# Performance work log

Hardware: AMD Instinct MI355X
Metric: run time of the kernel (lower is better)

The kernel has to match this reference:

```python
import jax, jax.numpy as jnp
import numpy as np

D_MODEL = 1024
D_STATE = 16
D_CONV = 4
EXPAND = 2
DT_RANK = 64
D_INNER = EXPAND * D_MODEL  # 2048
BATCH = 2
SEQ = 1024


def _silu(v):
    return v * jax.nn.sigmoid(v)


def setup_inputs() -> dict:
    key = jax.random.key(0)
    ks = jax.random.split(key, 8)
    x = jax.random.normal(ks[0], (BATCH, SEQ, D_MODEL), dtype=jnp.float32)
    W_in = jax.random.normal(ks[1], (2 * D_INNER, D_MODEL), dtype=jnp.float32) * (D_MODEL ** -0.5)
    conv_w = jax.random.normal(ks[2], (D_INNER, 1, D_CONV), dtype=jnp.float32) * (D_CONV ** -0.5)
    conv_b = jnp.zeros((D_INNER,), dtype=jnp.float32)
    W_x = jax.random.normal(ks[3], (DT_RANK + 2 * D_STATE, D_INNER), dtype=jnp.float32) * (D_INNER ** -0.5)
    W_dt = jax.random.uniform(ks[4], (D_INNER, DT_RANK), minval=-(DT_RANK ** -0.5), maxval=DT_RANK ** -0.5, dtype=jnp.float32)
    # dt bias init: inverse-softplus of dt sampled log-uniform in [1e-3, 1e-1]
    dt = jnp.exp(jax.random.uniform(ks[5], (D_INNER,), dtype=jnp.float32) * (np.log(0.1) - np.log(0.001)) + np.log(0.001))
    dt = jnp.clip(dt, 1e-4)
    b_dt = dt + jnp.log(-jnp.expm1(-dt))
    # A_log init: log of 1..d_state tiled per channel (S4D-real)
    A_log = jnp.log(jnp.tile(jnp.arange(1, D_STATE + 1, dtype=jnp.float32), (D_INNER, 1)))
    D = jnp.ones((D_INNER,), dtype=jnp.float32)
    W_out = jax.random.normal(ks[6], (D_MODEL, D_INNER), dtype=jnp.float32) * (D_INNER ** -0.5)
    return {"x": x, "W_in": W_in, "conv_w": conv_w, "conv_b": conv_b, "W_x": W_x,
            "W_dt": W_dt, "b_dt": b_dt, "A_log": A_log, "D": D, "W_out": W_out}


def _selective_scan(u, dt, A, B_in, C_in, D):
    # u, dt: [B,L,d_inner]; B_in, C_in: [B,L,d_state]; A: [d_inner,d_state]; D: [d_inner]
    Bsz = u.shape[0]

    def step(h, inp):
        u_t, dt_t, B_t, C_t = inp  # [B,d_inner], [B,d_inner], [B,d_state], [B,d_state]
        dA = jnp.exp(dt_t[:, :, None] * A)                     # [B,d_inner,d_state]
        h = dA * h + dt_t[:, :, None] * B_t[:, None, :] * u_t[:, :, None]
        y = jnp.einsum('bds,bs->bd', h, C_t)
        return h, y

    h0 = jnp.zeros((Bsz, D_INNER, D_STATE), dtype=u.dtype)
    xs = (u.transpose(1, 0, 2), dt.transpose(1, 0, 2),
          B_in.transpose(1, 0, 2), C_in.transpose(1, 0, 2))
    _, ys = jax.lax.scan(step, h0, xs)                          # ys: [L,B,d_inner]
    return ys.transpose(1, 0, 2) + u * D


def reference(x, W_in, conv_w, conv_b, W_x, W_dt, b_dt, A_log, D, W_out):
    # in_proj and gate split
    xz = x @ W_in.T                                            # [B,T,2*d_inner]
    x_in, z = jnp.split(xz, 2, axis=-1)
    # depthwise causal conv1d (left-pad d_conv-1, same as pad-both + slice :T)
    xi = x_in.transpose(0, 2, 1)                               # [B,d_inner,T]
    conv = jax.lax.conv_general_dilated(xi, conv_w, window_strides=(1,),
                                        padding=[(D_CONV - 1, 0)],
                                        feature_group_count=D_INNER)
    x_act = _silu(conv + conv_b[None, :, None]).transpose(0, 2, 1)  # [B,T,d_inner]
    # dt / B / C projections
    dbc = x_act @ W_x.T
    dt_lr, B_in, C_in = jnp.split(dbc, [DT_RANK, DT_RANK + D_STATE], axis=-1)
    dt = jax.nn.softplus(dt_lr @ W_dt.T + b_dt)                # [B,T,d_inner]
    A = -jnp.exp(A_log)                                        # [d_inner,d_state]
    y = _selective_scan(x_act, dt, A, B_in, C_in, D)
    y = y * _silu(z)
    return y @ W_out.T
```

## Files before the change

kernel.cpp:

```cpp
#include <hip/hip_runtime.h>
#include <math.h>

#define D_MODEL 1024
#define D_STATE 16
#define D_CONV  4
#define DT_RANK 64
#define D_INNER 2048
#define BATCH   2
#define SEQ     1024
#define BT      (BATCH*SEQ)
#define KSPLIT  16

typedef int   v4i __attribute__((ext_vector_type(4)));
typedef float v4f __attribute__((ext_vector_type(4)));
typedef short s8v __attribute__((ext_vector_type(8)));
typedef unsigned short u16;

template<int BM, int BN, int BK, int TM, int TN, int EPI>
__launch_bounds__(256)
__global__ void gemm_nt(const float* __restrict__ A, int lda,
                        const float* __restrict__ B, int ldb,
                        float* __restrict__ C, int ldc,
                        int K, const float* __restrict__ bias) {
    constexpr int BX = BN / TN;
    constexpr int BY = BM / TM;
    constexpr int THREADS = BX * BY;

    __shared__ float As[BK][BM + 1];
    __shared__ float Bs[BK][BN + 1];

    const int tid = threadIdx.x;
    const int tx  = tid % BX;
    const int ty  = tid / BX;
    const int m0  = blockIdx.y * BM;
    const int n0  = blockIdx.x * BN;

    float acc[TM][TN] = {};

    for (int k0 = 0; k0 < K; k0 += BK) {
        #pragma unroll
        for (int l = 0; l < (BM * BK) / (THREADS * 4); ++l) {
            int idx = (tid + l * THREADS) * 4;
            int row = idx / BK, col = idx % BK;
            const float4 v = *reinterpret_cast<const float4*>(
                &A[(size_t)(m0 + row) * lda + k0 + col]);
            As[col + 0][row] = v.x; As[col + 1][row] = v.y;
            As[col + 2][row] = v.z; As[col + 3][row] = v.w;
        }
        #pragma unroll
        for (int l = 0; l < (BN * BK) / (THREADS * 4); ++l) {
            int idx = (tid + l * THREADS) * 4;
            int row = idx / BK, col = idx % BK;
            const float4 v = *reinterpret_cast<const float4*>(
                &B[(size_t)(n0 + row) * ldb + k0 + col]);
            Bs[col + 0][row] = v.x; Bs[col + 1][row] = v.y;
            Bs[col + 2][row] = v.z; Bs[col + 3][row] = v.w;
        }
        __syncthreads();

        #pragma unroll
        for (int kk = 0; kk < BK; ++kk) {
            float a[TM], b[TN];
            #pragma unroll
            for (int i = 0; i < TM; ++i) a[i] = As[kk][ty * TM + i];
            #pragma unroll
            for (int j = 0; j < TN; ++j) b[j] = Bs[kk][tx * TN + j];
            #pragma unroll
            for (int i = 0; i < TM; ++i)
                #pragma unroll
                for (int j = 0; j < TN; ++j)
                    acc[i][j] = fmaf(a[i], b[j], acc[i][j]);
        }
        __syncthreads();
    }

    #pragma unroll
    for (int i = 0; i < TM; ++i) {
        float* outp = &C[(size_t)(m0 + ty * TM + i) * ldc + n0 + tx * TN];
        float vals[4];
        #pragma unroll
        for (int j = 0; j < TN; ++j) {
            float val = acc[i][j];
            if (EPI == 1) {
                val += bias[n0 + tx * TN + j];
                val = (val > 20.f) ? val : log1pf(expf(val));
            }
            vals[j] = val;
        }
        float4 v;
        v.x = vals[0]; v.y = vals[1]; v.z = vals[2]; v.w = vals[3];
        *reinterpret_cast<float4*>(outp) = v;
    }
}

template<int BM, int BN, int BK, int TM, int TN>
__launch_bounds__(128)
__global__ void gemm_nt_splitk(const float* __restrict__ A, int lda,
                               const float* __restrict__ B, int ldb,
                               float* __restrict__ part, int N, int kchunk) {
    constexpr int BX = BN / TN;
    constexpr int BY = BM / TM;
    constexpr int THREADS = BX * BY;

    __shared__ float As[BK][BM + 1];
    __shared__ float Bs[BK][BN + 1];

    const int tid = threadIdx.x;
    const int tx  = tid % BX;
    const int ty  = tid / BX;
    const int m0  = blockIdx.y * BM;
    const int n0  = blockIdx.x * BN;
    const int kb  = blockIdx.z * kchunk;

    float acc[TM][TN] = {};

    for (int k0 = kb; k0 < kb + kchunk; k0 += BK) {
        #pragma unroll
        for (int l = 0; l < (BM * BK) / (THREADS * 4); ++l) {
            int idx = (tid + l * THREADS) * 4;
            int row = idx / BK, col = idx % BK;
            const float4 v = *reinterpret_cast<const float4*>(
                &A[(size_t)(m0 + row) * lda + k0 + col]);
            As[col + 0][row] = v.x; As[col + 1][row] = v.y;
            As[col + 2][row] = v.z; As[col + 3][row] = v.w;
        }
        #pragma unroll
        for (int l = 0; l < (BN * BK) / (THREADS * 4); ++l) {
            int idx = (tid + l * THREADS) * 4;
            int row = idx / BK, col = idx % BK;
            const float4 v = *reinterpret_cast<const float4*>(
                &B[(size_t)(n0 + row) * ldb + k0 + col]);
            Bs[col + 0][row] = v.x; Bs[col + 1][row] = v.y;
            Bs[col + 2][row] = v.z; Bs[col + 3][row] = v.w;
        }
        __syncthreads();

        #pragma unroll
        for (int kk = 0; kk < BK; ++kk) {
            float a[TM], b[TN];
            #pragma unroll
            for (int i = 0; i < TM; ++i) a[i] = As[kk][ty * TM + i];
            #pragma unroll
            for (int j = 0; j < TN; ++j) b[j] = Bs[kk][tx * TN + j];
            #pragma unroll
            for (int i = 0; i < TM; ++i)
                #pragma unroll
                for (int j = 0; j < TN; ++j)
                    acc[i][j] = fmaf(a[i], b[j], acc[i][j]);
        }
        __syncthreads();
    }

    float* base = part + (size_t)blockIdx.z * BT * N;
    #pragma unroll
    for (int i = 0; i < TM; ++i) {
        float* outp = &base[(size_t)(m0 + ty * TM + i) * N + n0 + tx * TN];
        float4 v;
        v.x = acc[i][0]; v.y = acc[i][1]; v.z = acc[i][2]; v.w = acc[i][3];
        *reinterpret_cast<float4*>(outp) = v;
    }
}

__global__ void reduce_splitk(const float* __restrict__ part,
                              float* __restrict__ outp, int n) {
    const int idx = blockIdx.x * 256 + threadIdx.x;
    if (idx >= n) return;
    float s = 0.f;
    #pragma unroll
    for (int kc = 0; kc < KSPLIT; ++kc)
        s += part[(size_t)kc * n + idx];
    outp[idx] = s;
}

__device__ __forceinline__ u16 rne_bf16(float x) {
    unsigned int u = __float_as_uint(x);
    unsigned int r = u + 0x7FFFu + ((u >> 16) & 1u);
    return (u16)(r >> 16);
}
__device__ __forceinline__ float bf2f(u16 h) {
    return __uint_as_float((unsigned int)h << 16);
}

__global__ void prep_kernel(const float* __restrict__ x,
                            const float* __restrict__ Win,
                            const float* __restrict__ Wout,
                            u16* __restrict__ xh,
                            u16* __restrict__ winh, u16* __restrict__ wouth) {
    const size_t M2 = 2u * 1024u * 1024u;
    size_t i = ((size_t)blockIdx.x * 256 + threadIdx.x) * 8;
    const float* src;
    u16* dst;
    size_t j;
    if (i < M2)            { src = x;    dst = xh;    j = i; }
    else if (i < 3 * M2)   { src = Win;  dst = winh;  j = i - M2; }
    else                   { src = Wout; dst = wouth; j = i - 3 * M2; }
    float4 a = *reinterpret_cast<const float4*>(&src[j]);
    float4 b = *reinterpret_cast<const float4*>(&src[j + 4]);
    float xs[8] = {a.x, a.y, a.z, a.w, b.x, b.y, b.z, b.w};
    unsigned int hw[4];
    #pragma unroll
    for (int q = 0; q < 4; ++q)
        hw[q] = (unsigned int)rne_bf16(xs[2*q]) | ((unsigned int)rne_bf16(xs[2*q+1]) << 16);
    *reinterpret_cast<v4i*>(&dst[j]) = *reinterpret_cast<v4i*>(hw);
}

template<int BM, int BN, int WM, int WN, int CBF16>
__launch_bounds__(256)
__global__ void gemm_bf16(const u16* __restrict__ Ahi, int lda,
                          const u16* __restrict__ Bhi, int ldb,
                          void* __restrict__ Cp, int ldc, int K) {
    constexpr int ACH = BM / 64;
    constexpr int BCH = BN / 64;
    constexpr int WMF = WM / 16;
    constexpr int WNF = WN / 16;
    constexpr int SA  = BM * 40;
    constexpr int SB  = BN * 40;
    constexpr int BUFSZ = SA + SB;
    constexpr int WCOLS = BN / WN;

    __shared__ u16 smem[2 * BUFSZ];

    const int tid  = threadIdx.x;
    const int lane = tid & 63;
    const int wave = tid >> 6;
    const int wr   = wave / WCOLS, wc = wave % WCOLS;
    const int m0   = blockIdx.y * BM, n0 = blockIdx.x * BN;

    size_t aBase[ACH]; int aW[ACH];
    #pragma unroll
    for (int q = 0; q < ACH; ++q) {
        int c = tid + q * 256, row = c >> 2, slot = c & 3;
        aBase[q] = (size_t)(m0 + row) * lda + slot * 8;
        aW[q] = row * 40 + slot * 8;
    }
    size_t bBase[BCH]; int bW[BCH];
    #pragma unroll
    for (int q = 0; q < BCH; ++q) {
        int c = tid + q * 256, row = c >> 2, slot = c & 3;
        bBase[q] = (size_t)(n0 + row) * ldb + slot * 8;
        bW[q] = row * 40 + slot * 8;
    }

    const int fr = lane & 15;
    const int fk = (lane >> 4) * 8;
    const int fq = lane >> 4;
    int aOff[WMF], bOff[WNF];
    #pragma unroll
    for (int i = 0; i < WMF; ++i) aOff[i] = (wr * WM + i * 16 + fr) * 40 + fk;
    #pragma unroll
    for (int j = 0; j < WNF; ++j) bOff[j] = (wc * WN + j * 16 + fr) * 40 + fk;

    v4f acc[WMF][WNF];
    #pragma unroll
    for (int i = 0; i < WMF; ++i)
        #pragma unroll
        for (int j = 0; j < WNF; ++j)
            acc[i][j] = (v4f)0.f;

    v4i rA[ACH], rB[BCH];

    auto loadg = [&](int k0) {
        #pragma unroll
        for (int q = 0; q < ACH; ++q)
            rA[q] = *reinterpret_cast<const v4i*>(Ahi + aBase[q] + k0);
        #pragma unroll
        for (int q = 0; q < BCH; ++q)
            rB[q] = *reinterpret_cast<const v4i*>(Bhi + bBase[q] + k0);
    };
    auto writelds = [&](u16* buf) {
        #pragma unroll
        for (int q = 0; q < ACH; ++q)
            *reinterpret_cast<v4i*>(&buf[aW[q]]) = rA[q];
        #pragma unroll
        for (int q = 0; q < BCH; ++q)
            *reinterpret_cast<v4i*>(&buf[SA + bW[q]]) = rB[q];
    };

    const int NK = K / 32;
    loadg(0);
    writelds(smem);
    if (NK > 1) loadg(32);
    __syncthreads();

    for (int k = 0; k < NK; ++k) {
        u16* cur = smem + (k & 1) * BUFSZ;
        if (k + 1 < NK) {
            writelds(smem + ((k + 1) & 1) * BUFSZ);
            if (k + 2 < NK) loadg((k + 2) * 32);
        }

        s8v ah[WMF];
        #pragma unroll
        for (int i = 0; i < WMF; ++i)
            ah[i] = *reinterpret_cast<const s8v*>(&cur[aOff[i]]);
        #pragma unroll
        for (int j = 0; j < WNF; ++j) {
            const s8v bh = *reinterpret_cast<const s8v*>(&cur[SA + bOff[j]]);
            #pragma unroll
            for (int i = 0; i < WMF; ++i)
                acc[i][j] = __builtin_amdgcn_mfma_f32_16x16x32_bf16(ah[i], bh, acc[i][j], 0, 0, 0);
        }
        __syncthreads();
    }

    #pragma unroll
    for (int i = 0; i < WMF; ++i) {
        const int row = m0 + wr * WM + i * 16 + fq * 4;
        #pragma unroll
        for (int j = 0; j < WNF; ++j) {
            const int col = n0 + wc * WN + j * 16 + fr;
            #pragma unroll
            for (int r = 0; r < 4; ++r) {
                if constexpr (CBF16) {
                    ((u16*)Cp)[(size_t)(row + r) * ldc + col] = rne_bf16(acc[i][j][r]);
                } else {
                    ((float*)Cp)[(size_t)(row + r) * ldc + col] = acc[i][j][r];
                }
            }
        }
    }
}

template<int INBF16>
__global__ void conv_silu_kernel(const void* __restrict__ x_in, int xld,
                                 const float* __restrict__ w,
                                 const float* __restrict__ b,
                                 float* __restrict__ x_act) {
    const int idx = blockIdx.x * blockDim.x + threadIdx.x;
    const int ch4 = (idx * 4) % D_INNER;
    const int m   = (idx * 4) / D_INNER;
    const int t   = m % SEQ;

    float4 wrow[4];
    #pragma unroll
    for (int c = 0; c < 4; ++c)
        wrow[c] = *reinterpret_cast<const float4*>(&w[(ch4 + c) * D_CONV]);
    float4 acc = *reinterpret_cast<const float4*>(&b[ch4]);

    #pragma unroll
    for (int j = 0; j < D_CONV; ++j) {
        const int tt = t - (D_CONV - 1) + j;
        if (tt >= 0) {
            float xi[4];
            if (INBF16) {
                const ushort4 v = *reinterpret_cast<const ushort4*>(
                    &((const u16*)x_in)[(size_t)(m - (D_CONV - 1) + j) * xld + ch4]);
                xi[0] = bf2f(v.x); xi[1] = bf2f(v.y);
                xi[2] = bf2f(v.z); xi[3] = bf2f(v.w);
            } else {
                const float4 v = *reinterpret_cast<const float4*>(
                    &((const float*)x_in)[(size_t)(m - (D_CONV - 1) + j) * xld + ch4]);
                xi[0] = v.x; xi[1] = v.y; xi[2] = v.z; xi[3] = v.w;
            }
            acc.x = fmaf(((const float*)&wrow[0])[j], xi[0], acc.x);
            acc.y = fmaf(((const float*)&wrow[1])[j], xi[1], acc.y);
            acc.z = fmaf(((const float*)&wrow[2])[j], xi[2], acc.z);
            acc.w = fmaf(((const float*)&wrow[3])[j], xi[3], acc.w);
        }
    }
    acc.x = acc.x / (1.f + __expf(-acc.x));
    acc.y = acc.y / (1.f + __expf(-acc.y));
    acc.z = acc.z / (1.f + __expf(-acc.z));
    acc.w = acc.w / (1.f + __expf(-acc.w));
    *reinterpret_cast<float4*>(&x_act[(size_t)idx * 4]) = acc;
}

template<int NC>
__launch_bounds__(256)
__global__ void scan_part1(const float* __restrict__ dt,
                           const float* __restrict__ x_act,
                           const float* __restrict__ dbc,
                           const float* __restrict__ A_log,
                           float* __restrict__ P, float* __restrict__ F) {
    constexpr int CL = SEQ / NC;
    __shared__ float Bsh[CL][D_STATE];
    const int tid = threadIdx.x;
    const int d = blockIdx.x * 256 + tid;
    const int c = blockIdx.y;
    const int b = blockIdx.z;
    const int mbase = b * SEQ + c * CL;

    {
        const int s = tid & 15, t0 = tid >> 4;
        #pragma unroll
        for (int q = 0; q < CL / 16; ++q)
            Bsh[t0 + 16 * q][s] = dbc[(size_t)(mbase + t0 + 16 * q) * 96 + DT_RANK + s];
    }
    float A[16];
    #pragma unroll
    for (int q = 0; q < 4; ++q) {
        float4 v = *reinterpret_cast<const float4*>(&A_log[d * 16 + q * 4]);
        A[q*4+0] = -__expf(v.x); A[q*4+1] = -__expf(v.y);
        A[q*4+2] = -__expf(v.z); A[q*4+3] = -__expf(v.w);
    }
    __syncthreads();

    float h[16] = {};
    float Pp[16];
    #pragma unroll
    for (int s = 0; s < 16; ++s) Pp[s] = 1.f;

    for (int t = 0; t < CL; ++t) {
        const int m = mbase + t;
        const float dtv = dt[(size_t)m * D_INNER + d];
        const float u   = x_act[(size_t)m * D_INNER + d];
        const float du  = dtv * u;
        float Bv[16];
        #pragma unroll
        for (int q = 0; q < 4; ++q) {
            float4 v = *reinterpret_cast<const float4*>(&Bsh[t][q * 4]);
            Bv[q*4+0] = v.x; Bv[q*4+1] = v.y; Bv[q*4+2] = v.z; Bv[q*4+3] = v.w;
        }
        #pragma unroll
        for (int s = 0; s < 16; ++s) {
            const float dA = __expf(dtv * A[s]);
            Pp[s] *= dA;
            h[s] = fmaf(dA, h[s], du * Bv[s]);
        }
    }
    const size_t base = ((size_t)(b * NC + c) * 16) * D_INNER + d;
    #pragma unroll
    for (int s = 0; s < 16; ++s) {
        P[base + (size_t)s * D_INNER] = Pp[s];
        F[base + (size_t)s * D_INNER] = h[s];
    }
}

template<int NC>
__launch_bounds__(256, 2)
__global__ void scan_combine(const float* __restrict__ P, float* F) {
    const int idx = blockIdx.x * 256 + threadIdx.x;
    const int d  = idx % D_INNER;
    const int bs = idx / D_INNER;
    const int b  = bs >> 4, s = bs & 15;
    const size_t base0 = ((size_t)b * NC * 16 + s) * D_INNER + d;
    const size_t cstep = (size_t)16 * D_INNER;

    float Pv[NC], Fv[NC];
    #pragma unroll
    for (int c = 0; c < NC; ++c) {
        Pv[c] = P[base0 + c * cstep];
        Fv[c] = F[base0 + c * cstep];
    }
    float G = 0.f;
    #pragma unroll
    for (int c = 0; c < NC; ++c) {
        const float f = Fv[c];
        Fv[c] = G;
        G = fmaf(Pv[c], G, f);
    }
    #pragma unroll
    for (int c = 0; c < NC; ++c)
        F[base0 + c * cstep] = Fv[c];
}

template<int NC, int ZBF16, int BF16OUT>
__launch_bounds__(256)
__global__ void scan_part2(const float* __restrict__ dt,
                           const float* __restrict__ x_act,
                           const float* __restrict__ dbc,
                           const float* __restrict__ A_log,
                           const float* __restrict__ Dp,
                           const float* __restrict__ Ginit,
                           const void* zp, int zld,
                           float* yf, u16* yh) {
    constexpr int CL = SEQ / NC;
    __shared__ float BCs[CL][32];
    const int tid = threadIdx.x;
    const int d = blockIdx.x * 256 + tid;
    const int c = blockIdx.y;
    const int b = blockIdx.z;
    const int mbase = b * SEQ + c * CL;

    {
        const int t0 = tid >> 3;
        const int j  = (tid & 7) * 4;
        if (t0 < CL) {
            float4 v = *reinterpret_cast<const float4*>(
                &dbc[(size_t)(mbase + t0) * 96 + DT_RANK + j]);
            *reinterpret_cast<float4*>(&BCs[t0][j]) = v;
        }
    }
    float A[16];
    #pragma unroll
    for (int q = 0; q < 4; ++q) {
        float4 v = *reinterpret_cast<const float4*>(&A_log[d * 16 + q * 4]);
        A[q*4+0] = -__expf(v.x); A[q*4+1] = -__expf(v.y);
        A[q*4+2] = -__expf(v.z); A[q*4+3] = -__expf(v.w);
    }
    float h[16];
    const size_t gbase = ((size_t)(b * NC + c) * 16) * D_INNER + d;
    #pragma unroll
    for (int s = 0; s < 16; ++s) h[s] = Ginit[gbase + (size_t)s * D_INNER];
    const float Dv = Dp[d];
    __syncthreads();

    for (int half = 0; half < 2; ++half) {
        const int tb = half * (CL / 2);
        float zreg[CL / 2];
        #pragma unroll
        for (int t = 0; t < CL / 2; ++t) {
            if (ZBF16)
                zreg[t] = bf2f(((const u16*)zp)[(size_t)(mbase + tb + t) * zld + d]);
            else
                zreg[t] = ((const float*)zp)[(size_t)(mbase + tb + t) * zld + d];
        }

        for (int t = 0; t < CL / 2; ++t) {
            const int m = mbase + tb + t;
            const float dtv = dt[(size_t)m * D_INNER + d];
            const float u   = x_act[(size_t)m * D_INNER + d];
            const float du  = dtv * u;
            float Bv[16], Cv[16];
            #pragma unroll
            for (int q = 0; q < 4; ++q) {
                float4 vb = *reinterpret_cast<const float4*>(&BCs[tb + t][q * 4]);
                float4 vc = *reinterpret_cast<const float4*>(&BCs[tb + t][16 + q * 4]);
                Bv[q*4+0] = vb.x; Bv[q*4+1] = vb.y; Bv[q*4+2] = vb.z; Bv[q*4+3] = vb.w;
                Cv[q*4+0] = vc.x; Cv[q*4+1] = vc.y; Cv[q*4+2] = vc.z; Cv[q*4+3] = vc.w;
            }
            float y0 = 0.f, y1 = 0.f;
            #pragma unroll
            for (int s = 0; s < 16; s += 2) {
                const float dA0 = __expf(dtv * A[s]);
                const float dA1 = __expf(dtv * A[s + 1]);
                h[s]     = fmaf(dA0, h[s],     du * Bv[s]);
                h[s + 1] = fmaf(dA1, h[s + 1], du * Bv[s + 1]);
                y0 = fmaf(h[s],     Cv[s],     y0);
                y1 = fmaf(h[s + 1], Cv[s + 1], y1);
            }
            float y = y0 + y1;
            y = fmaf(u, Dv, y);
            const float zv = zreg[t];
            const float g  = zv / (1.f + __expf(-zv));
            const float val = y * g;
            if (BF16OUT) {
                yh[(size_t)m * D_INNER + d] = rne_bf16(val);
            } else {
                yf[(size_t)m * D_INNER + d] = val;
            }
        }
    }
}

extern "C" void kernel_launch(void* const* d_in, const int* in_sizes, int n_in,
                              void* d_out, int out_size, void* d_ws, size_t ws_size,
                              hipStream_t stream) {
    const float* x      = (const float*)d_in[0];
    const float* W_in   = (const float*)d_in[1];
    const float* conv_w = (const float*)d_in[2];
    const float* conv_b = (const float*)d_in[3];
    const float* W_x    = (const float*)d_in[4];
    const float* W_dt   = (const float*)d_in[5];
    const float* b_dt   = (const float*)d_in[6];
    const float* A_log  = (const float*)d_in[7];
    const float* Dp     = (const float*)d_in[8];
    const float* W_out  = (const float*)d_in[9];
    float* out = (float*)d_out;

    const size_t M1 = 1024u * 1024u;
    const size_t fXACT = 4 * M1, fDBC = (size_t)BT * 96, fDT = 4 * M1;
    const size_t fPF32 = 2 * M1;
    const size_t fPF64 = 4 * M1;
    const size_t shorts = 20 * M1;
    const size_t need32 = (fXACT + fDBC + fDT + 2 * fPF32) * 4 + shorts * 2;
    const size_t need64 = (fXACT + fDBC + fDT + 2 * fPF64) * 4 + shorts * 2;

    if (ws_size >= need32) {
        const bool big = (ws_size >= need64);
        const size_t fPF = big ? fPF64 : fPF32;

        float* ws    = (float*)d_ws;
        float* x_act = ws;
        float* dbc   = x_act + fXACT;
        float* dtbuf = dbc   + fDBC;
        float* Pbuf  = dtbuf + fDT;
        float* Fbuf  = Pbuf  + fPF;
        u16* xh    = (u16*)(Fbuf + fPF);
        u16* winh  = xh    + 2 * M1;
        u16* wouth = winh  + 4 * M1;
        u16* xz    = wouth + 2 * M1;
        u16* yh    = xz    + 8 * M1;
        float* dbc_part = Pbuf;

        prep_kernel<<<dim3((8 * M1) / 2048), 256, 0, stream>>>(
            x, W_in, W_out, xh, winh, wouth);

        gemm_bf16<128, 128, 64, 64, 1><<<dim3(4096 / 128, BT / 128), 256, 0, stream>>>(
            xh, D_MODEL, winh, D_MODEL, xz, 4096, D_MODEL);

        conv_silu_kernel<1><<<dim3((BT * D_INNER) / 1024), 256, 0, stream>>>(
            xz, 4096, conv_w, conv_b, x_act);

        gemm_nt_splitk<64,32,16,4,4><<<dim3(96 / 32, BT / 64, KSPLIT), 128, 0, stream>>>(
            x_act, D_INNER, W_x, D_INNER, dbc_part, 96, D_INNER / KSPLIT);
        reduce_splitk<<<dim3((BT * 96 + 255) / 256), 256, 0, stream>>>(
            dbc_part, dbc, BT * 96);

        gemm_nt<64,64,16,4,4,1><<<dim3(D_INNER / 64, BT / 64), 256, 0, stream>>>(
            dbc, 96, W_dt, DT_RANK, dtbuf, D_INNER, DT_RANK, b_dt);

        if (big) {
            scan_part1<64><<<dim3(D_INNER / 256, 64, BATCH), 256, 0, stream>>>(
                dtbuf, x_act, dbc, A_log, Pbuf, Fbuf);
            scan_combine<64><<<dim3((BATCH * 16 * D_INNER) / 256), 256, 0, stream>>>(
                Pbuf, Fbuf);
            scan_part2<64, 1, 1><<<dim3(D_INNER / 256, 64, BATCH), 256, 0, stream>>>(
                dtbuf, x_act, dbc, A_log, Dp, Fbuf, xz + D_INNER, 4096,
                nullptr, yh);
        } else {
            scan_part1<32><<<dim3(D_INNER / 256, 32, BATCH), 256, 0, stream>>>(
                dtbuf, x_act, dbc, A_log, Pbuf, Fbuf);
            scan_combine<32><<<dim3((BATCH * 16 * D_INNER) / 256), 256, 0, stream>>>(
                Pbuf, Fbuf);
            scan_part2<32, 1, 1><<<dim3(D_INNER / 256, 32, BATCH), 256, 0, stream>>>(
                dtbuf, x_act, dbc, A_log, Dp, Fbuf, xz + D_INNER, 4096,
                nullptr, yh);
        }

        gemm_bf16<64, 128, 32, 64, 0><<<dim3(D_MODEL / 128, BT / 64), 256, 0, stream>>>(
            yh, D_INNER, wouth, D_INNER, out, D_MODEL, D_INNER);
    } else {
        float* ws    = (float*)d_ws;
        float* x_in  = ws;
        float* z     = x_in  + (size_t)BT * D_INNER;
        float* x_act = z     + (size_t)BT * D_INNER;
        float* dbc   = x_act + (size_t)BT * D_INNER;
        float* Pbuf  = dbc   + (size_t)BT * 96;
        float* Fbuf  = Pbuf  + (size_t)BATCH * 32 * 16 * D_INNER;
        float* dtbuf = x_in;
        float* yf    = z;

        gemm_nt<64,64,16,4,4,0><<<dim3(D_INNER/64, BT/64), 256, 0, stream>>>(
            x, D_MODEL, W_in, D_MODEL, x_in, D_INNER, D_MODEL, nullptr);
        gemm_nt<64,64,16,4,4,0><<<dim3(D_INNER/64, BT/64), 256, 0, stream>>>(
            x, D_MODEL, W_in + (size_t)D_INNER * D_MODEL, D_MODEL, z, D_INNER, D_MODEL, nullptr);
        conv_silu_kernel<0><<<dim3((BT * D_INNER) / 1024), 256, 0, stream>>>(
            x_in, D_INNER, conv_w, conv_b, x_act);
        gemm_nt<64,32,16,4,4,0><<<dim3(96/32, BT/64), 128, 0, stream>>>(
            x_act, D_INNER, W_x, D_INNER, dbc, 96, D_INNER, nullptr);
        gemm_nt<64,64,16,4,4,1><<<dim3(D_INNER/64, BT/64), 256, 0, stream>>>(
            dbc, 96, W_dt, DT_RANK, dtbuf, D_INNER, DT_RANK, b_dt);
        scan_part1<32><<<dim3(D_INNER/256, 32, BATCH), 256, 0, stream>>>(
            dtbuf, x_act, dbc, A_log, Pbuf, Fbuf);
        scan_combine<32><<<dim3((BATCH * 16 * D_INNER) / 256), 256, 0, stream>>>(
            Pbuf, Fbuf);
        scan_part2<32, 0, 0><<<dim3(D_INNER/256, 32, BATCH), 256, 0, stream>>>(
            dtbuf, x_act, dbc, A_log, Dp, Fbuf, z, D_INNER, yf, nullptr);
        gemm_nt<64,64,16,4,4,0><<<dim3(D_MODEL/64, BT/64), 256, 0, stream>>>(
            yf, D_INNER, W_out, D_INNER, out, D_MODEL, D_INNER, nullptr);
    }
}
```

Baseline: 180.6 us.

## Fuse depthwise conv+SiLU into dbc split-K GEMM and scan kernels

Removes the standalone conv_silu kernel and the fp32 x_act buffer on the main path. The causal conv and SiLU are recomputed from the bf16 xz activations inside the dbc split-K GEMM's A-tile load and inside both scan passes, which keep a rolling 3-tap window per channel. This trades one write and several reads of a 16 MB fp32 intermediate for redundant conv arithmetic and extra strided bf16 loads. The fallback path also gains an apparently stray split-K launch that writes into scratch space.

```diff
diff --git a/kernel.cpp b/kernel.cpp
--- a/kernel.cpp
+++ b/kernel.cpp
@@ -16,6 +16,15 @@
 typedef short s8v __attribute__((ext_vector_type(8)));
 typedef unsigned short u16;
 
+__device__ __forceinline__ u16 rne_bf16(float x) {
+    unsigned int u = __float_as_uint(x);
+    unsigned int r = u + 0x7FFFu + ((u >> 16) & 1u);
+    return (u16)(r >> 16);
+}
+__device__ __forceinline__ float bf2f(u16 h) {
+    return __uint_as_float((unsigned int)h << 16);
+}
+
 template<int BM, int BN, int BK, int TM, int TN, int EPI>
 __launch_bounds__(256)
 __global__ void gemm_nt(const float* __restrict__ A, int lda,
@@ -93,6 +102,97 @@
     }
 }
 
+__launch_bounds__(128)
+__global__ void gemm_dbc_splitk(const u16* __restrict__ xz, int xld,
+                                const float* __restrict__ convw,
+                                const float* __restrict__ convb,
+                                const float* __restrict__ B, int ldb,
+                                float* __restrict__ part, int N, int kchunk) {
+    constexpr int BM = 64, BN = 32, BK = 16, TM = 4, TN = 4;
+    constexpr int BX = BN / TN;
+    constexpr int BY = BM / TM;
+    constexpr int THREADS = BX * BY;
+
+    __shared__ float As[BK][BM + 1];
+    __shared__ float Bs[BK][BN + 1];
+
+    const int tid = threadIdx.x;
+    const int tx  = tid % BX;
+    const int ty  = tid / BX;
+    const int m0  = blockIdx.y * BM;
+    const int n0  = blockIdx.x * BN;
+    const int kb  = blockIdx.z * kchunk;
+
+    float acc[TM][TN] = {};
+
+    for (int k0 = kb; k0 < kb + kchunk; k0 += BK) {
+        #pragma unroll
+        for (int l = 0; l < (BM * BK) / (THREADS * 4); ++l) {
+            int idx = (tid + l * THREADS) * 4;
+            int row = idx / BK, col = idx % BK;
+            const int m  = m0 + row;
+            const int t  = m & (SEQ - 1);
+            const int ch = k0 + col;
+            float4 w0 = *reinterpret_cast<const float4*>(&convw[(ch + 0) * 4]);
+            float4 w1 = *reinterpret_cast<const float4*>(&convw[(ch + 1) * 4]);
+            float4 w2 = *reinterpret_cast<const float4*>(&convw[(ch + 2) * 4]);
+            float4 w3 = *reinterpret_cast<const float4*>(&convw[(ch + 3) * 4]);
+            float4 bb = *reinterpret_cast<const float4*>(&convb[ch]);
+            float a0 = bb.x, a1 = bb.y, a2 = bb.z, a3 = bb.w;
+            #pragma unroll
+            for (int j = 0; j < D_CONV; ++j) {
+                const int tt = t - (D_CONV - 1) + j;
+                if (tt >= 0) {
+                    const ushort4 xv = *reinterpret_cast<const ushort4*>(
+                        &xz[(size_t)(m - (D_CONV - 1) + j) * xld + ch]);
+                    a0 = fmaf(((const float*)&w0)[j], bf2f(xv.x), a0);
+                    a1 = fmaf(((const float*)&w1)[j], bf2f(xv.y), a1);
+                    a2 = fmaf(((const float*)&w2)[j], bf2f(xv.z), a2);
+                    a3 = fmaf(((const float*)&w3)[j], bf2f(xv.w), a3);
+                }
+            }
+            As[col + 0][row] = a0 / (1.f + __expf(-a0));
+            As[col + 1][row] = a1 / (1.f + __expf(-a1));
+            As[col + 2][row] = a2 / (1.f + __expf(-a2));
+            As[col + 3][row] = a3 / (1.f + __expf(-a3));
+        }
+        #pragma unroll
+        for (int l = 0; l < (BN * BK) / (THREADS * 4); ++l) {
+            int idx = (tid + l * THREADS) * 4;
+            int row = idx / BK, col = idx % BK;
+            const float4 v = *reinterpret_cast<const float4*>(
+                &B[(size_t)(n0 + row) * ldb + k0 + col]);
+            Bs[col + 0][row] = v.x; Bs[col + 1][row] = v.y;
+            Bs[col + 2][row] = v.z; Bs[col + 3][row] = v.w;
+        }
+        __syncthreads();
+
+        #pragma unroll
+        for (int kk = 0; kk < BK; ++kk) {
+            float a[TM], b[TN];
+            #pragma unroll
+            for (int i = 0; i < TM; ++i) a[i] = As[kk][ty * TM + i];
+            #pragma unroll
+            for (int j = 0; j < TN; ++j) b[j] = Bs[kk][tx * TN + j];
+            #pragma unroll
+            for (int i = 0; i < TM; ++i)
+                #pragma unroll
+                for (int j = 0; j < TN; ++j)
+                    acc[i][j] = fmaf(a[i], b[j], acc[i][j]);
+        }
+        __syncthreads();
+    }
+
+    float* base = part + (size_t)blockIdx.z * BT * N;
+    #pragma unroll
+    for (int i = 0; i < TM; ++i) {
+        float* outp = &base[(size_t)(m0 + ty * TM + i) * N + n0 + tx * TN];
+        float4 v;
+        v.x = acc[i][0]; v.y = acc[i][1]; v.z = acc[i][2]; v.w = acc[i][3];
+        *reinterpret_cast<float4*>(outp) = v;
+    }
+}
+
 template<int BM, int BN, int BK, int TM, int TN>
 __launch_bounds__(128)
 __global__ void gemm_nt_splitk(const float* __restrict__ A, int lda,
@@ -170,15 +270,6 @@
     for (int kc = 0; kc < KSPLIT; ++kc)
         s += part[(size_t)kc * n + idx];
     outp[idx] = s;
-}
-
-__device__ __forceinline__ u16 rne_bf16(float x) {
-    unsigned int u = __float_as_uint(x);
-    unsigned int r = u + 0x7FFFu + ((u >> 16) & 1u);
-    return (u16)(r >> 16);
-}
-__device__ __forceinline__ float bf2f(u16 h) {
-    return __uint_as_float((unsigned int)h << 16);
 }
 
 __global__ void prep_kernel(const float* __restrict__ x,
@@ -321,8 +412,7 @@
     }
 }
 
-template<int INBF16>
-__global__ void conv_silu_kernel(const void* __restrict__ x_in, int xld,
+__global__ void conv_silu_kernel(const float* __restrict__ x_in, int xld,
                                  const float* __restrict__ w,
                                  const float* __restrict__ b,
                                  float* __restrict__ x_act) {
@@ -341,21 +431,12 @@
     for (int j = 0; j < D_CONV; ++j) {
         const int tt = t - (D_CONV - 1) + j;
         if (tt >= 0) {
-            float xi[4];
-            if (INBF16) {
-                const ushort4 v = *reinterpret_cast<const ushort4*>(
-                    &((const u16*)x_in)[(size_t)(m - (D_CONV - 1) + j) * xld + ch4]);
-                xi[0] = bf2f(v.x); xi[1] = bf2f(v.y);
-                xi[2] = bf2f(v.z); xi[3] = bf2f(v.w);
-            } else {
-                const float4 v = *reinterpret_cast<const float4*>(
-                    &((const float*)x_in)[(size_t)(m - (D_CONV - 1) + j) * xld + ch4]);
-                xi[0] = v.x; xi[1] = v.y; xi[2] = v.z; xi[3] = v.w;
-            }
-            acc.x = fmaf(((const float*)&wrow[0])[j], xi[0], acc.x);
-            acc.y = fmaf(((const float*)&wrow[1])[j], xi[1], acc.y);
-            acc.z = fmaf(((const float*)&wrow[2])[j], xi[2], acc.z);
-            acc.w = fmaf(((const float*)&wrow[3])[j], xi[3], acc.w);
+            const float4 v = *reinterpret_cast<const float4*>(
+                &x_in[(size_t)(m - (D_CONV - 1) + j) * xld + ch4]);
+            acc.x = fmaf(((const float*)&wrow[0])[j], v.x, acc.x);
+            acc.y = fmaf(((const float*)&wrow[1])[j], v.y, acc.y);
+            acc.z = fmaf(((const float*)&wrow[2])[j], v.z, acc.z);
+            acc.w = fmaf(((const float*)&wrow[3])[j], v.w, acc.w);
         }
     }
     acc.x = acc.x / (1.f + __expf(-acc.x));
@@ -365,10 +446,12 @@
     *reinterpret_cast<float4*>(&x_act[(size_t)idx * 4]) = acc;
 }
 
-template<int NC>
+template<int NC, int FUSE>
 __launch_bounds__(256)
 __global__ void scan_part1(const float* __restrict__ dt,
-                           const float* __restrict__ x_act,
+                           const void* __restrict__ xin, int xld,
+                           const float* __restrict__ convw,
+                           const float* __restrict__ convb,
                            const float* __restrict__ dbc,
                            const float* __restrict__ A_log,
                            float* __restrict__ P, float* __restrict__ F) {
@@ -393,6 +476,18 @@
         A[q*4+0] = -__expf(v.x); A[q*4+1] = -__expf(v.y);
         A[q*4+2] = -__expf(v.z); A[q*4+3] = -__expf(v.w);
     }
+
+    float4 cw; float cb;
+    float xw0 = 0.f, xw1 = 0.f, xw2 = 0.f;
+    if constexpr (FUSE) {
+        cw = *reinterpret_cast<const float4*>(&convw[d * 4]);
+        cb = convb[d];
+        const u16* xzp = (const u16*)xin;
+        const int t0g = c * CL;
+        if (t0g - 3 >= 0) xw0 = bf2f(xzp[(size_t)(mbase - 3) * xld + d]);
+        if (t0g - 2 >= 0) xw1 = bf2f(xzp[(size_t)(mbase - 2) * xld + d]);
+        if (t0g - 1 >= 0) xw2 = bf2f(xzp[(size_t)(mbase - 1) * xld + d]);
+    }
     __syncthreads();
 
     float h[16] = {};
@@ -403,7 +498,19 @@
     for (int t = 0; t < CL; ++t) {
         const int m = mbase + t;
         const float dtv = dt[(size_t)m * D_INNER + d];
-        const float u   = x_act[(size_t)m * D_INNER + d];
+        float u;
+        if constexpr (FUSE) {
+            const float xc = bf2f(((const u16*)xin)[(size_t)m * xld + d]);
+            float a = cb;
+            a = fmaf(cw.x, xw0, a);
+            a = fmaf(cw.y, xw1, a);
+            a = fmaf(cw.z, xw2, a);
+            a = fmaf(cw.w, xc,  a);
+            u = a / (1.f + __expf(-a));
+            xw0 = xw1; xw1 = xw2; xw2 = xc;
+        } else {
+            u = ((const float*)xin)[(size_t)m * xld + d];
+        }
         const float du  = dtv * u;
         float Bv[16];
         #pragma unroll
@@ -454,10 +561,12 @@
         F[base0 + c * cstep] = Fv[c];
 }
 
-template<int NC, int ZBF16, int BF16OUT>
+template<int NC, int FUSE, int ZBF16, int BF16OUT>
 __launch_bounds__(256)
 __global__ void scan_part2(const float* __restrict__ dt,
-                           const float* __restrict__ x_act,
+                           const void* __restrict__ xin, int xld,
+                           const float* __restrict__ convw,
+                           const float* __restrict__ convb,
                            const float* __restrict__ dbc,
                            const float* __restrict__ A_log,
                            const float* __restrict__ Dp,
@@ -493,6 +602,18 @@
     #pragma unroll
     for (int s = 0; s < 16; ++s) h[s] = Ginit[gbase + (size_t)s * D_INNER];
     const float Dv = Dp[d];
+
+    float4 cw; float cb;
+    float xw0 = 0.f, xw1 = 0.f, xw2 = 0.f;
+    if constexpr (FUSE) {
+        cw = *reinterpret_cast<const float4*>(&convw[d * 4]);
+        cb = convb[d];
+        const u16* xzp = (const u16*)xin;
+        const int t0g = c * CL;
+        if (t0g - 3 >= 0) xw0 = bf2f(xzp[(size_t)(mbase - 3) * xld + d]);
+        if (t0g - 2 >= 0) xw1 = bf2f(xzp[(size_t)(mbase - 2) * xld + d]);
+        if (t0g - 1 >= 0) xw2 = bf2f(xzp[(size_t)(mbase - 1) * xld + d]);
+    }
     __syncthreads();
 
     for (int half = 0; half < 2; ++half) {
@@ -509,7 +630,19 @@
         for (int t = 0; t < CL / 2; ++t) {
             const int m = mbase + tb + t;
             const float dtv = dt[(size_t)m * D_INNER + d];
-            const float u   = x_act[(size_t)m * D_INNER + d];
+            float u;
+            if constexpr (FUSE) {
+                const float xc = bf2f(((const u16*)xin)[(size_t)m * xld + d]);
+                float a = cb;
+                a = fmaf(cw.x, xw0, a);
+                a = fmaf(cw.y, xw1, a);
+                a = fmaf(cw.z, xw2, a);
+                a = fmaf(cw.w, xc,  a);
+                u = a / (1.f + __expf(-a));
+                xw0 = xw1; xw1 = xw2; xw2 = xc;
+            } else {
+                u = ((const float*)xin)[(size_t)m * xld + d];
+            }
             const float du  = dtv * u;
             float Bv[16], Cv[16];
             #pragma unroll
@@ -559,20 +692,19 @@
     float* out = (float*)d_out;
 
     const size_t M1 = 1024u * 1024u;
-    const size_t fXACT = 4 * M1, fDBC = (size_t)BT * 96, fDT = 4 * M1;
+    const size_t fDBC = (size_t)BT * 96, fDT = 4 * M1;
     const size_t fPF32 = 2 * M1;
     const size_t fPF64 = 4 * M1;
     const size_t shorts = 20 * M1;
-    const size_t need32 = (fXACT + fDBC + fDT + 2 * fPF32) * 4 + shorts * 2;
-    const size_t need64 = (fXACT + fDBC + fDT + 2 * fPF64) * 4 + shorts * 2;
+    const size_t need32 = (fDBC + fDT + 2 * fPF32) * 4 + shorts * 2;
+    const size_t need64 = (fDBC + fDT + 2 * fPF64) * 4 + shorts * 2;
 
     if (ws_size >= need32) {
         const bool big = (ws_size >= need64);
         const size_t fPF = big ? fPF64 : fPF32;
 
         float* ws    = (float*)d_ws;
-        float* x_act = ws;
-        float* dbc   = x_act + fXACT;
+        float* dbc   = ws;
         float* dtbuf = dbc   + fDBC;
         float* Pbuf  = dtbuf + fDT;
         float* Fbuf  = Pbuf  + fPF;
@@ -589,11 +721,8 @@
         gemm_bf16<128, 128, 64, 64, 1><<<dim3(4096 / 128, BT / 128), 256, 0, stream>>>(
             xh, D_MODEL, winh, D_MODEL, xz, 4096, D_MODEL);
 
-        conv_silu_kernel<1><<<dim3((BT * D_INNER) / 1024), 256, 0, stream>>>(
-            xz, 4096, conv_w, conv_b, x_act);
-
-        gemm_nt_splitk<64,32,16,4,4><<<dim3(96 / 32, BT / 64, KSPLIT), 128, 0, stream>>>(
-            x_act, D_INNER, W_x, D_INNER, dbc_part, 96, D_INNER / KSPLIT);
+        gemm_dbc_splitk<<<dim3(96 / 32, BT / 64, KSPLIT), 128, 0, stream>>>(
+            xz, 4096, conv_w, conv_b, W_x, D_INNER, dbc_part, 96, D_INNER / KSPLIT);
         reduce_splitk<<<dim3((BT * 96 + 255) / 256), 256, 0, stream>>>(
             dbc_part, dbc, BT * 96);
 
@@ -601,21 +730,21 @@
             dbc, 96, W_dt, DT_RANK, dtbuf, D_INNER, DT_RANK, b_dt);
 
         if (big) {
-            scan_part1<64><<<dim3(D_INNER / 256, 64, BATCH), 256, 0, stream>>>(
-                dtbuf, x_act, dbc, A_log, Pbuf, Fbuf);
+            scan_part1<64, 1><<<dim3(D_INNER / 256, 64, BATCH), 256, 0, stream>>>(
+                dtbuf, xz, 4096, conv_w, conv_b, dbc, A_log, Pbuf, Fbuf);
             scan_combine<64><<<dim3((BATCH * 16 * D_INNER) / 256), 256, 0, stream>>>(
                 Pbuf, Fbuf);
-            scan_part2<64, 1, 1><<<dim3(D_INNER / 256, 64, BATCH), 256, 0, stream>>>(
-                dtbuf, x_act, dbc, A_log, Dp, Fbuf, xz + D_INNER, 4096,
-                nullptr, yh);
+            scan_part2<64, 1, 1, 1><<<dim3(D_INNER / 256, 64, BATCH), 256, 0, stream>>>(
+                dtbuf, xz, 4096, conv_w, conv_b, dbc, A_log, Dp, Fbuf,
+                xz + D_INNER, 4096, nullptr, yh);
         } else {
-            scan_part1<32><<<dim3(D_INNER / 256, 32, BATCH), 256, 0, stream>>>(
-                dtbuf, x_act, dbc, A_log, Pbuf, Fbuf);
+            scan_part1<32, 1><<<dim3(D_INNER / 256, 32, BATCH), 256, 0, stream>>>(
+                dtbuf, xz, 4096, conv_w, conv_b, dbc, A_log, Pbuf, Fbuf);
             scan_combine<32><<<dim3((BATCH * 16 * D_INNER) / 256), 256, 0, stream>>>(
                 Pbuf, Fbuf);
-            scan_part2<32, 1, 1><<<dim3(D_INNER / 256, 32, BATCH), 256, 0, stream>>>(
-                dtbuf, x_act, dbc, A_log, Dp, Fbuf, xz + D_INNER, 4096,
-                nullptr, yh);
+            scan_part2<32, 1, 1, 1><<<dim3(D_INNER / 256, 32, BATCH), 256, 0, stream>>>(
+                dtbuf, xz, 4096, conv_w, conv_b, dbc, A_log, Dp, Fbuf,
+                xz + D_INNER, 4096, nullptr, yh);
         }
 
         gemm_bf16<64, 128, 32, 64, 0><<<dim3(D_MODEL / 128, BT / 64), 256, 0, stream>>>(
@@ -635,18 +764,21 @@
             x, D_MODEL, W_in, D_MODEL, x_in, D_INNER, D_MODEL, nullptr);
         gemm_nt<64,64,16,4,4,0><<<dim3(D_INNER/64, BT/64), 256, 0, stream>>>(
             x, D_MODEL, W_in + (size_t)D_INNER * D_MODEL, D_MODEL, z, D_INNER, D_MODEL, nullptr);
-        conv_silu_kernel<0><<<dim3((BT * D_INNER) / 1024), 256, 0, stream>>>(
+        conv_silu_kernel<<<dim3((BT * D_INNER) / 1024), 256, 0, stream>>>(
             x_in, D_INNER, conv_w, conv_b, x_act);
+        gemm_nt_splitk<64,32,16,4,4><<<dim3(96/32, BT/64, KSPLIT), 128, 0, stream>>>(
+            x_act, D_INNER, W_x, D_INNER, Fbuf + (size_t)BATCH*32*16*D_INNER, 96, D_INNER / KSPLIT);
         gemm_nt<64,32,16,4,4,0><<<dim3(96/32, BT/64), 128, 0, stream>>>(
             x_act, D_INNER, W_x, D_INNER, dbc, 96, D_INNER, nullptr);
         gemm_nt<64,64,16,4,4,1><<<dim3(D_INNER/64, BT/64), 256, 0, stream>>>(
             dbc, 96, W_dt, DT_RANK, dtbuf, D_INNER, DT_RANK, b_dt);
-        scan_part1<32><<<dim3(D_INNER/256, 32, BATCH), 256, 0, stream>>>(
-            dtbuf, x_act, dbc, A_log, Pbuf, Fbuf);
+        scan_part1<32, 0><<<dim3(D_INNER/256, 32, BATCH), 256, 0, stream>>>(
+            dtbuf, x_act, D_INNER, nullptr, nullptr, dbc, A_log, Pbuf, Fbuf);
         scan_combine<32><<<dim3((BATCH * 16 * D_INNER) / 256), 256, 0, stream>>>(
             Pbuf, Fbuf);
-        scan_part2<32, 0, 0><<<dim3(D_INNER/256, 32, BATCH), 256, 0, stream>>>(
-            dtbuf, x_act, dbc, A_log, Dp, Fbuf, z, D_INNER, yf, nullptr);
+        scan_part2<32, 0, 0, 0><<<dim3(D_INNER/256, 32, BATCH), 256, 0, stream>>>(
+            dtbuf, x_act, D_INNER, nullptr, nullptr, dbc, A_log, Dp, Fbuf,
+            z, D_INNER, yf, nullptr);
         gemm_nt<64,64,16,4,4,0><<<dim3(D_MODEL/64, BT/64), 256, 0, stream>>>(
             yf, D_INNER, W_out, D_INNER, out, D_MODEL, D_INNER, nullptr);
     }
```

New measurement: 184.4 us. +2.1%, slower.

## Run dt projection on bf16 MFMA GEMM and fuse conv+SiLU into scan kernels

Applied to the files above, without the earlier changes.

Converts W_dt to bf16 in the prep kernel and has the split-K reduce emit a bf16 copy of the dt low-rank input, so the dt projection runs on the MFMA bf16 GEMM with bias+softplus fused in its epilogue. The scan kernels now recompute the causal depthwise conv and SiLU from the bf16 xz buffer instead of loading fp32 x_act, halving that read traffic. This adds bf16 rounding to the dt path and duplicates conv/SiLU arithmetic in both scan passes; the separate conv kernel is still needed for the W_x projection.

```diff
diff --git a/kernel.cpp b/kernel.cpp
--- a/kernel.cpp
+++ b/kernel.cpp
@@ -16,6 +16,15 @@
 typedef short s8v __attribute__((ext_vector_type(8)));
 typedef unsigned short u16;
 
+__device__ __forceinline__ u16 rne_bf16(float x) {
+    unsigned int u = __float_as_uint(x);
+    unsigned int r = u + 0x7FFFu + ((u >> 16) & 1u);
+    return (u16)(r >> 16);
+}
+__device__ __forceinline__ float bf2f(u16 h) {
+    return __uint_as_float((unsigned int)h << 16);
+}
+
 template<int BM, int BN, int BK, int TM, int TN, int EPI>
 __launch_bounds__(256)
 __global__ void gemm_nt(const float* __restrict__ A, int lda,
@@ -162,7 +171,8 @@
 }
 
 __global__ void reduce_splitk(const float* __restrict__ part,
-                              float* __restrict__ outp, int n) {
+                              float* __restrict__ outp,
+                              u16* __restrict__ dtin, int n) {
     const int idx = blockIdx.x * 256 + threadIdx.x;
     if (idx >= n) return;
     float s = 0.f;
@@ -170,22 +180,20 @@
     for (int kc = 0; kc < KSPLIT; ++kc)
         s += part[(size_t)kc * n + idx];
     outp[idx] = s;
-}
-
-__device__ __forceinline__ u16 rne_bf16(float x) {
-    unsigned int u = __float_as_uint(x);
-    unsigned int r = u + 0x7FFFu + ((u >> 16) & 1u);
-    return (u16)(r >> 16);
-}
-__device__ __forceinline__ float bf2f(u16 h) {
-    return __uint_as_float((unsigned int)h << 16);
+    if (dtin) {
+        const int col = idx % 96;
+        if (col < DT_RANK)
+            dtin[(size_t)(idx / 96) * DT_RANK + col] = rne_bf16(s);
+    }
 }
 
 __global__ void prep_kernel(const float* __restrict__ x,
                             const float* __restrict__ Win,
                             const float* __restrict__ Wout,
+                            const float* __restrict__ Wdt,
                             u16* __restrict__ xh,
-                            u16* __restrict__ winh, u16* __restrict__ wouth) {
+                            u16* __restrict__ winh, u16* __restrict__ wouth,
+                            u16* __restrict__ wdth) {
     const size_t M2 = 2u * 1024u * 1024u;
     size_t i = ((size_t)blockIdx.x * 256 + threadIdx.x) * 8;
     const float* src;
@@ -193,7 +201,8 @@
     size_t j;
     if (i < M2)            { src = x;    dst = xh;    j = i; }
     else if (i < 3 * M2)   { src = Win;  dst = winh;  j = i - M2; }
-    else                   { src = Wout; dst = wouth; j = i - 3 * M2; }
+    else if (i < 4 * M2)   { src = Wout; dst = wouth; j = i - 3 * M2; }
+    else                   { src = Wdt;  dst = wdth;  j = i - 4 * M2; }
     float4 a = *reinterpret_cast<const float4*>(&src[j]);
     float4 b = *reinterpret_cast<const float4*>(&src[j + 4]);
     float xs[8] = {a.x, a.y, a.z, a.w, b.x, b.y, b.z, b.w};
@@ -204,11 +213,12 @@
     *reinterpret_cast<v4i*>(&dst[j]) = *reinterpret_cast<v4i*>(hw);
 }
 
-template<int BM, int BN, int WM, int WN, int CBF16>
+template<int BM, int BN, int WM, int WN, int CBF16, int EPI>
 __launch_bounds__(256)
 __global__ void gemm_bf16(const u16* __restrict__ Ahi, int lda,
                           const u16* __restrict__ Bhi, int ldb,
-                          void* __restrict__ Cp, int ldc, int K) {
+                          void* __restrict__ Cp, int ldc, int K,
+                          const float* __restrict__ bias) {
     constexpr int ACH = BM / 64;
     constexpr int BCH = BN / 64;
     constexpr int WMF = WM / 16;
@@ -311,10 +321,15 @@
             const int col = n0 + wc * WN + j * 16 + fr;
             #pragma unroll
             for (int r = 0; r < 4; ++r) {
+                float val = acc[i][j][r];
+                if constexpr (EPI == 1) {
+                    val += bias[col];
+                    val = (val > 20.f) ? val : log1pf(expf(val));
+                }
                 if constexpr (CBF16) {
-                    ((u16*)Cp)[(size_t)(row + r) * ldc + col] = rne_bf16(acc[i][j][r]);
+                    ((u16*)Cp)[(size_t)(row + r) * ldc + col] = rne_bf16(val);
                 } else {
-                    ((float*)Cp)[(size_t)(row + r) * ldc + col] = acc[i][j][r];
+                    ((float*)Cp)[(size_t)(row + r) * ldc + col] = val;
                 }
             }
         }
@@ -365,10 +380,12 @@
     *reinterpret_cast<float4*>(&x_act[(size_t)idx * 4]) = acc;
 }
 
-template<int NC>
+template<int NC, int FUSE>
 __launch_bounds__(256)
 __global__ void scan_part1(const float* __restrict__ dt,
-                           const float* __restrict__ x_act,
+                           const void* __restrict__ xin, int xld,
+                           const float* __restrict__ convw,
+                           const float* __restrict__ convb,
                            const float* __restrict__ dbc,
                            const float* __restrict__ A_log,
                            float* __restrict__ P, float* __restrict__ F) {
@@ -393,6 +410,18 @@
         A[q*4+0] = -__expf(v.x); A[q*4+1] = -__expf(v.y);
         A[q*4+2] = -__expf(v.z); A[q*4+3] = -__expf(v.w);
     }
+
+    float4 cw; float cb;
+    float xw0 = 0.f, xw1 = 0.f, xw2 = 0.f;
+    if constexpr (FUSE) {
+        cw = *reinterpret_cast<const float4*>(&convw[d * 4]);
+        cb = convb[d];
+        const u16* xzp = (const u16*)xin;
+        const int t0g = c * CL;
+        if (t0g - 3 >= 0) xw0 = bf2f(xzp[(size_t)(mbase - 3) * xld + d]);
+        if (t0g - 2 >= 0) xw1 = bf2f(xzp[(size_t)(mbase - 2) * xld + d]);
+        if (t0g - 1 >= 0) xw2 = bf2f(xzp[(size_t)(mbase - 1) * xld + d]);
+    }
     __syncthreads();
 
     float h[16] = {};
@@ -403,7 +432,19 @@
     for (int t = 0; t < CL; ++t) {
         const int m = mbase + t;
         const float dtv = dt[(size_t)m * D_INNER + d];
-        const float u   = x_act[(size_t)m * D_INNER + d];
+        float u;
+        if constexpr (FUSE) {
+            const float xc = bf2f(((const u16*)xin)[(size_t)m * xld + d]);
+            float a = cb;
+            a = fmaf(cw.x, xw0, a);
+            a = fmaf(cw.y, xw1, a);
+            a = fmaf(cw.z, xw2, a);
+            a = fmaf(cw.w, xc,  a);
+            u = a / (1.f + __expf(-a));
+            xw0 = xw1; xw1 = xw2; xw2 = xc;
+        } else {
+            u = ((const float*)xin)[(size_t)m * xld + d];
+        }
         const float du  = dtv * u;
         float Bv[16];
         #pragma unroll
@@ -454,10 +495,12 @@
         F[base0 + c * cstep] = Fv[c];
 }
 
-template<int NC, int ZBF16, int BF16OUT>
+template<int NC, int FUSE, int ZBF16, int BF16OUT>
 __launch_bounds__(256)
 __global__ void scan_part2(const float* __restrict__ dt,
-                           const float* __restrict__ x_act,
+                           const void* __restrict__ xin, int xld,
+                           const float* __restrict__ convw,
+                           const float* __restrict__ convb,
                            const float* __restrict__ dbc,
                            const float* __restrict__ A_log,
                            const float* __restrict__ Dp,
@@ -493,6 +536,18 @@
     #pragma unroll
     for (int s = 0; s < 16; ++s) h[s] = Ginit[gbase + (size_t)s * D_INNER];
     const float Dv = Dp[d];
+
+    float4 cw; float cb;
+    float xw0 = 0.f, xw1 = 0.f, xw2 = 0.f;
+    if constexpr (FUSE) {
+        cw = *reinterpret_cast<const float4*>(&convw[d * 4]);
+        cb = convb[d];
+        const u16* xzp = (const u16*)xin;
+        const int t0g = c * CL;
+        if (t0g - 3 >= 0) xw0 = bf2f(xzp[(size_t)(mbase - 3) * xld + d]);
+        if (t0g - 2 >= 0) xw1 = bf2f(xzp[(size_t)(mbase - 2) * xld + d]);
+        if (t0g - 1 >= 0) xw2 = bf2f(xzp[(size_t)(mbase - 1) * xld + d]);
+    }
     __syncthreads();
 
     for (int half = 0; half < 2; ++half) {
@@ -509,7 +564,19 @@
         for (int t = 0; t < CL / 2; ++t) {
             const int m = mbase + tb + t;
             const float dtv = dt[(size_t)m * D_INNER + d];
-            const float u   = x_act[(size_t)m * D_INNER + d];
+            float u;
+            if constexpr (FUSE) {
+                const float xc = bf2f(((const u16*)xin)[(size_t)m * xld + d]);
+                float a = cb;
+                a = fmaf(cw.x, xw0, a);
+                a = fmaf(cw.y, xw1, a);
+                a = fmaf(cw.z, xw2, a);
+                a = fmaf(cw.w, xc,  a);
+                u = a / (1.f + __expf(-a));
+                xw0 = xw1; xw1 = xw2; xw2 = xc;
+            } else {
+                u = ((const float*)xin)[(size_t)m * xld + d];
+            }
             const float du  = dtv * u;
             float Bv[16], Cv[16];
             #pragma unroll
@@ -562,7 +629,8 @@
     const size_t fXACT = 4 * M1, fDBC = (size_t)BT * 96, fDT = 4 * M1;
     const size_t fPF32 = 2 * M1;
     const size_t fPF64 = 4 * M1;
-    const size_t shorts = 20 * M1;
+    const size_t WDT = (size_t)D_INNER * DT_RANK;
+    const size_t shorts = 20 * M1 + 2 * WDT;
     const size_t need32 = (fXACT + fDBC + fDT + 2 * fPF32) * 4 + shorts * 2;
     const size_t need64 = (fXACT + fDBC + fDT + 2 * fPF64) * 4 + shorts * 2;
 
@@ -579,15 +647,17 @@
         u16* xh    = (u16*)(Fbuf + fPF);
         u16* winh  = xh    + 2 * M1;
         u16* wouth = winh  + 4 * M1;
-        u16* xz    = wouth + 2 * M1;
+        u16* wdth  = wouth + 2 * M1;
+        u16* xz    = wdth  + WDT;
         u16* yh    = xz    + 8 * M1;
+        u16* dtin  = yh    + 4 * M1;
         float* dbc_part = Pbuf;
 
-        prep_kernel<<<dim3((8 * M1) / 2048), 256, 0, stream>>>(
-            x, W_in, W_out, xh, winh, wouth);
-
-        gemm_bf16<128, 128, 64, 64, 1><<<dim3(4096 / 128, BT / 128), 256, 0, stream>>>(
-            xh, D_MODEL, winh, D_MODEL, xz, 4096, D_MODEL);
+        prep_kernel<<<dim3((8 * M1 + WDT) / 2048), 256, 0, stream>>>(
+            x, W_in, W_out, W_dt, xh, winh, wouth, wdth);
+
+        gemm_bf16<128, 128, 64, 64, 1, 0><<<dim3(4096 / 128, BT / 128), 256, 0, stream>>>(
+            xh, D_MODEL, winh, D_MODEL, xz, 4096, D_MODEL, nullptr);
 
         conv_silu_kernel<1><<<dim3((BT * D_INNER) / 1024), 256, 0, stream>>>(
             xz, 4096, conv_w, conv_b, x_act);
@@ -595,31 +665,31 @@
         gemm_nt_splitk<64,32,16,4,4><<<dim3(96 / 32, BT / 64, KSPLIT), 128, 0, stream>>>(
             x_act, D_INNER, W_x, D_INNER, dbc_part, 96, D_INNER / KSPLIT);
         reduce_splitk<<<dim3((BT * 96 + 255) / 256), 256, 0, stream>>>(
-            dbc_part, dbc, BT * 96);
-
-        gemm_nt<64,64,16,4,4,1><<<dim3(D_INNER / 64, BT / 64), 256, 0, stream>>>(
-            dbc, 96, W_dt, DT_RANK, dtbuf, D_INNER, DT_RANK, b_dt);
+            dbc_part, dbc, dtin, BT * 96);
+
+        gemm_bf16<64, 128, 32, 64, 0, 1><<<dim3(D_INNER / 128, BT / 64), 256, 0, stream>>>(
+            dtin, DT_RANK, wdth, DT_RANK, dtbuf, D_INNER, DT_RANK, b_dt);
 
         if (big) {
-            scan_part1<64><<<dim3(D_INNER / 256, 64, BATCH), 256, 0, stream>>>(
-                dtbuf, x_act, dbc, A_log, Pbuf, Fbuf);
+            scan_part1<64, 1><<<dim3(D_INNER / 256, 64, BATCH), 256, 0, stream>>>(
+                dtbuf, xz, 4096, conv_w, conv_b, dbc, A_log, Pbuf, Fbuf);
             scan_combine<64><<<dim3((BATCH * 16 * D_INNER) / 256), 256, 0, stream>>>(
                 Pbuf, Fbuf);
-            scan_part2<64, 1, 1><<<dim3(D_INNER / 256, 64, BATCH), 256, 0, stream>>>(
-                dtbuf, x_act, dbc, A_log, Dp, Fbuf, xz + D_INNER, 4096,
-                nullptr, yh);
+            scan_part2<64, 1, 1, 1><<<dim3(D_INNER / 256, 64, BATCH), 256, 0, stream>>>(
+                dtbuf, xz, 4096, conv_w, conv_b, dbc, A_log, Dp, Fbuf,
+                xz + D_INNER, 4096, nullptr, yh);
         } else {
-            scan_part1<32><<<dim3(D_INNER / 256, 32, BATCH), 256, 0, stream>>>(
-                dtbuf, x_act, dbc, A_log, Pbuf, Fbuf);
+            scan_part1<32, 1><<<dim3(D_INNER / 256, 32, BATCH), 256, 0, stream>>>(
+                dtbuf, xz, 4096, conv_w, conv_b, dbc, A_log, Pbuf, Fbuf);
             scan_combine<32><<<dim3((BATCH * 16 * D_INNER) / 256), 256, 0, stream>>>(
                 Pbuf, Fbuf);
-            scan_part2<32, 1, 1><<<dim3(D_INNER / 256, 32, BATCH), 256, 0, stream>>>(
-                dtbuf, x_act, dbc, A_log, Dp, Fbuf, xz + D_INNER, 4096,
-                nullptr, yh);
-        }
-
-        gemm_bf16<64, 128, 32, 64, 0><<<dim3(D_MODEL / 128, BT / 64), 256, 0, stream>>>(
-            yh, D_INNER, wouth, D_INNER, out, D_MODEL, D_INNER);
+            scan_part2<32, 1, 1, 1><<<dim3(D_INNER / 256, 32, BATCH), 256, 0, stream>>>(
+                dtbuf, xz, 4096, conv_w, conv_b, dbc, A_log, Dp, Fbuf,
+                xz + D_INNER, 4096, nullptr, yh);
+        }
+
+        gemm_bf16<64, 128, 32, 64, 0, 0><<<dim3(D_MODEL / 128, BT / 64), 256, 0, stream>>>(
+            yh, D_INNER, wouth, D_INNER, out, D_MODEL, D_INNER, nullptr);
     } else {
         float* ws    = (float*)d_ws;
         float* x_in  = ws;
@@ -641,12 +711,13 @@
             x_act, D_INNER, W_x, D_INNER, dbc, 96, D_INNER, nullptr);
         gemm_nt<64,64,16,4,4,1><<<dim3(D_INNER/64, BT/64), 256, 0, stream>>>(
             dbc, 96, W_dt, DT_RANK, dtbuf, D_INNER, DT_RANK, b_dt);
-        scan_part1<32><<<dim3(D_INNER/256, 32, BATCH), 256, 0, stream>>>(
-            dtbuf, x_act, dbc, A_log, Pbuf, Fbuf);
+        scan_part1<32, 0><<<dim3(D_INNER/256, 32, BATCH), 256, 0, stream>>>(
+            dtbuf, x_act, D_INNER, nullptr, nullptr, dbc, A_log, Pbuf, Fbuf);
         scan_combine<32><<<dim3((BATCH * 16 * D_INNER) / 256), 256, 0, stream>>>(
             Pbuf, Fbuf);
-        scan_part2<32, 0, 0><<<dim3(D_INNER/256, 32, BATCH), 256, 0, stream>>>(
-            dtbuf, x_act, dbc, A_log, Dp, Fbuf, z, D_INNER, yf, nullptr);
+        scan_part2<32, 0, 0, 0><<<dim3(D_INNER/256, 32, BATCH), 256, 0, stream>>>(
+            dtbuf, x_act, D_INNER, nullptr, nullptr, dbc, A_log, Dp, Fbuf,
+            z, D_INNER, yf, nullptr);
         gemm_nt<64,64,16,4,4,0><<<dim3(D_MODEL/64, BT/64), 256, 0, stream>>>(
             yf, D_INNER, W_out, D_INNER, out, D_MODEL, D_INNER, nullptr);
     }
```

New measurement: 181.3 us, median of 2. No clear change (+0.4%).
